# Optimization experiments

Hardware: AMD Instinct MI355X
Metric: run time of the kernel (lower is better)

## Reference

```python
import jax, jax.numpy as jnp
import numpy as np

EMB = 512
HEADS = 8
HEAD_DIM = EMB // HEADS
GN_EPS = 1e-6
THETA_SCALE = 10000.0


def _multiply_by_i(x):
    # interleave: out[..., 2i] = -x[..., 2i+1], out[..., 2i+1] = x[..., 2i]
    return jnp.stack((-x[..., 1::2], x[..., ::2]), axis=-1).reshape(x.shape)


def _theta_shift(x, sin, cos):
    return x * cos + _multiply_by_i(x) * sin


def setup_inputs() -> dict:
    key = jax.random.key(0)
    ks = jax.random.split(key, 13)
    B, N, E = 2, 2048, EMB

    def xavier(k, out_dim, in_dim):
        std = (2.0 / (out_dim + in_dim)) ** 0.5
        return std * jax.random.normal(k, (out_dim, in_dim), dtype=jnp.float32)

    return {
        "query": jax.random.normal(ks[0], (B, N, E), dtype=jnp.float32),
        "k": jax.random.normal(ks[1], (B, N, E), dtype=jnp.float32),
        "v": jax.random.normal(ks[2], (B, N, E), dtype=jnp.float32),
        "Wq": xavier(ks[3], E, E), "bq": jnp.zeros((E,), jnp.float32),
        "Wk": xavier(ks[4], E, E), "bk": jnp.zeros((E,), jnp.float32),
        "Wv": xavier(ks[5], E, E), "bv": jnp.zeros((E,), jnp.float32),
        "Wg": xavier(ks[6], E, E), "bg": jnp.zeros((E,), jnp.float32),
        "Wo": xavier(ks[7], E, E), "bo": jnp.zeros((E,), jnp.float32),
    }


def reference(query, k, v, Wq, bq, Wk, bk, Wv, bv, Wg, bg, Wo, bo):
    B, N, E = query.shape
    H, D = HEADS, E // HEADS

    def proj(x, W, b):  # torch Linear: x @ W.T + b, then split heads -> [b h n d]
        return (x @ W.T + b).reshape(B, N, H, D).transpose(0, 2, 1, 3)

    q = proj(query, Wq, bq)
    kk = proj(k, Wk, bk)
    vv = proj(v, Wv, bv)

    # rotary-style theta shift; thetas repeated pairwise [t0,t0,t1,t1,...]
    thetas = jnp.repeat(1.0 / THETA_SCALE ** jnp.linspace(0.0, 1.0, D // 2), 2)
    angles = jnp.arange(N, dtype=jnp.float32)[:, None] * thetas[None, :]  # [n d]
    sin = jnp.sin(angles)[None, None]
    cos = jnp.cos(angles)[None, None]
    q = _theta_shift(q, sin, cos)
    kk = _theta_shift(kk, sin, cos)

    # decay-masked retention (softmax-free)
    gammas = 1.0 - jnp.exp(jnp.linspace(np.log(1 / 32), np.log(1 / 512), H)).astype(jnp.float32)
    pos = jnp.arange(N)
    dist = jnp.abs(pos[:, None] - pos[None, :]).astype(jnp.float32)
    causal = pos[:, None] >= pos[None, :]
    decay_mask = jnp.where(causal[None], gammas[:, None, None] ** dist[None], 0.0)  # [h n s]

    kk = kk / (D ** 0.5)
    sim = jnp.einsum('bhnd,bhsd->bhns', q, kk) * decay_mask[None]  # [b h n n]
    ret = jnp.einsum('bhns,bhsd->bhnd', sim, vv)

    # GroupNorm(groups=H, channels=H, affine=False) over (b n) samples -> per-(b,h,n) norm over d
    mean = ret.mean(axis=-1, keepdims=True)
    var = ret.var(axis=-1, keepdims=True)
    ret = (ret - mean) / jnp.sqrt(var + GN_EPS)

    ret = ret.transpose(0, 2, 1, 3).reshape(B, N, E)
    gate = jax.nn.silu(query @ Wg.T + bg)
    out = (ret * gate) @ Wo.T + bo
    return out
```

## Files before the change

kernel.cpp:

```cpp
#include <hip/hip_runtime.h>
#include <math.h>

typedef float f32x4 __attribute__((ext_vector_type(4)));
typedef short s16x8 __attribute__((ext_vector_type(8)));
typedef short s16x4 __attribute__((ext_vector_type(4)));

__device__ __forceinline__ short f2bf(float f) {
    unsigned u = __builtin_bit_cast(unsigned, f);
    unsigned r = u + 0x7FFFu + ((u >> 16) & 1u);
    return (short)(r >> 16);
}
__device__ __forceinline__ float bf2f(short h) {
    return __builtin_bit_cast(float, ((unsigned)(unsigned short)h) << 16);
}
__device__ __forceinline__ unsigned pack2(short a, short b) {
    return (unsigned)(unsigned short)a | ((unsigned)(unsigned short)b << 16);
}

__device__ __forceinline__ void split16v(const float* __restrict__ p,
                                         short* __restrict__ h,
                                         short* __restrict__ l) {
    f32x4 a0 = *(const f32x4*)(p);
    f32x4 a1 = *(const f32x4*)(p + 4);
    f32x4 a2 = *(const f32x4*)(p + 8);
    f32x4 a3 = *(const f32x4*)(p + 12);
    #pragma unroll
    for (int i = 0; i < 4; ++i) {
        short t0;
        t0 = f2bf(a0[i]); h[i]      = t0; l[i]      = f2bf(a0[i] - bf2f(t0));
        t0 = f2bf(a1[i]); h[4 + i]  = t0; l[4 + i]  = f2bf(a1[i] - bf2f(t0));
        t0 = f2bf(a2[i]); h[8 + i]  = t0; l[8 + i]  = f2bf(a2[i] - bf2f(t0));
        t0 = f2bf(a3[i]); h[12 + i] = t0; l[12 + i] = f2bf(a3[i] - bf2f(t0));
    }
}

__device__ __forceinline__ void gload16(const void* g, void* l) {
    __builtin_amdgcn_global_load_lds(
        (const __attribute__((address_space(1))) unsigned int*)g,
        (__attribute__((address_space(3))) unsigned int*)l,
        16, 0, 0);
}

__global__ __launch_bounds__(256) void presplit_kernel(
    const float* __restrict__ W0, const float* __restrict__ W1,
    const float* __restrict__ W2, const float* __restrict__ W3,
    const float* __restrict__ W4,
    const float* __restrict__ X0, const float* __restrict__ X1,
    const float* __restrict__ X2,
    short* __restrict__ Wsp, short* __restrict__ Xsp,
    float2* __restrict__ SC)
{
    const int blk = blockIdx.x;
    const int t = threadIdx.x;
    short hbuf[16], lbuf[16];
    if (blk < 256) {
        const int w = blk >> 6, bi = blk & 63;
        const float* src = (w == 0) ? W0 : (w == 1) ? W1 : (w == 2) ? W2 : W3;
        const int idx = (bi * 256 + t) * 16;
        const int row = idx >> 9, k0 = idx & 511;
        const int ntile = row >> 7, r = row & 127;
        const int kstep = k0 >> 5, kk0 = k0 & 31;
        const int s = (r & 3) << 4;
        split16v(src + idx, hbuf, lbuf);
        short* hp = Wsp + (long)w * 524288 + (ntile * 16 + kstep) * 8192 + r * 32;
        short* lp = hp + 4096;
        const int oA = ((2 * kk0) ^ s) >> 1;
        const int oB = ((2 * kk0 + 16) ^ s) >> 1;
        *(s16x8*)(hp + oA) = *(s16x8*)(hbuf);
        *(s16x8*)(hp + oB) = *(s16x8*)(hbuf + 8);
        *(s16x8*)(lp + oA) = *(s16x8*)(lbuf);
        *(s16x8*)(lp + oB) = *(s16x8*)(lbuf + 8);
    } else if (blk < 320) {
        const int bi = blk - 256;
        const int idx = (bi * 256 + t) * 16;
        short* hi = Wsp + (long)4 * 524288;
        short* lo = hi + 262144;
        split16v(W4 + idx, hbuf, lbuf);
        *(s16x8*)(hi + idx)     = *(s16x8*)(hbuf);
        *(s16x8*)(hi + idx + 8) = *(s16x8*)(hbuf + 8);
        *(s16x8*)(lo + idx)     = *(s16x8*)(lbuf);
        *(s16x8*)(lo + idx + 8) = *(s16x8*)(lbuf + 8);
    } else if (blk < 1856) {
        const int b2 = blk - 320;
        const int x = b2 >> 9, bi = b2 & 511;
        const float* src = (x == 0) ? X0 : (x == 1) ? X1 : X2;
        const int idx = (bi * 256 + t) * 16;
        const int row = idx >> 9, k0 = idx & 511;
        const int mtile = row >> 6, r = row & 63;
        const int kstep = k0 >> 5, kk0 = k0 & 31;
        const int s = (r & 3) << 4;
        split16v(src + idx, hbuf, lbuf);
        short* hp = Xsp + (long)x * 4194304 + (mtile * 16 + kstep) * 4096 + r * 32;
        short* lp = hp + 2048;
        const int oA = ((2 * kk0) ^ s) >> 1;
        const int oB = ((2 * kk0 + 16) ^ s) >> 1;
        *(s16x8*)(hp + oA) = *(s16x8*)(hbuf);
        *(s16x8*)(hp + oB) = *(s16x8*)(hbuf + 8);
        *(s16x8*)(lp + oA) = *(s16x8*)(lbuf);
        *(s16x8*)(lp + oB) = *(s16x8*)(lbuf + 8);
    } else {
        const int gid = (blk - 1856) * 256 + t;
        const int pos = gid >> 5, pp = gid & 31;
        const float theta = powf(10000.0f, -(float)pp * (1.0f / 31.0f));
        const float ang = (float)pos * theta;
        SC[gid] = make_float2(cosf(ang), sinf(ang));
    }
}

__global__ __launch_bounds__(512, 4) void projqkvg_kernel(
    const short* __restrict__ Xsp, const short* __restrict__ Wsp,
    const float* __restrict__ bq, const float* __restrict__ bk,
    const float* __restrict__ bv, const float* __restrict__ bg,
    const float2* __restrict__ SC,
    short* __restrict__ Qh, short* __restrict__ Ql,
    short* __restrict__ Kh, short* __restrict__ Vth,
    float* __restrict__ G)
{
    __shared__ __align__(16) short SB[36864];

    const int fid = blockIdx.x + 4 * (blockIdx.y + 64 * blockIdx.z);
    const int mtile = fid & 63;
    const int rr = fid >> 6;
    const int mode = rr & 3;
    const int ntile = rr >> 2;
    const int m0 = mtile * 64, n0 = ntile * 128;

    const int xi = (mode == 1) ? 1 : (mode == 2) ? 2 : 0;
    const float* bias = (mode == 0) ? bq : (mode == 1) ? bk
                       : (mode == 2) ? bv : bg;

    const int t = threadIdx.x, lane = t & 63, wv = t >> 6;
    const int wm = wv >> 2, wn = wv & 3;
    const int quad = lane >> 4, l15 = lane & 15;

    const short* Xblk = Xsp + (long)xi * 4194304 + (long)mtile * 16 * 4096;
    const short* Wblk = Wsp + (long)mode * 524288 + (long)ntile * 16 * 8192;

    const int c0 = wv * 3;
    const short* gs[3];
    int gstp[3];
    #pragma unroll
    for (int i = 0; i < 3; ++i) {
        const int c = c0 + i;
        const bool isx = (c < 8);
        gs[i]   = isx ? (Xblk + c * 512 + lane * 8)
                      : (Wblk + (c - 8) * 512 + lane * 8);
        gstp[i] = isx ? 4096 : 8192;
    }

    auto STAGE = [&](int stg, int ks) {
        char* dstb = (char*)SB + stg * 24576 + c0 * 1024;
        #pragma unroll
        for (int i = 0; i < 3; ++i)
            gload16(gs[i] + ks * gstp[i], dstb + i * 1024);
    };

    const int sxw = (l15 & 3) << 4;
    int aoff[2], boff[2];
    #pragma unroll
    for (int s2 = 0; s2 < 2; ++s2)
        aoff[s2] = (wm * 32 + s2 * 16 + l15) * 64 + ((quad * 16) ^ sxw);
    #pragma unroll
    for (int s2 = 0; s2 < 2; ++s2)
        boff[s2] = 8192 + (wn * 32 + s2 * 16 + l15) * 64 + ((quad * 16) ^ sxw);

    f32x4 acc[2][2];
    #pragma unroll
    for (int i = 0; i < 2; ++i)
        #pragma unroll
        for (int j = 0; j < 2; ++j)
            acc[i][j] = (f32x4){0.f, 0.f, 0.f, 0.f};

    STAGE(0, 0);
    STAGE(1, 1);
    asm volatile("s_waitcnt vmcnt(3)" ::: "memory");
    __builtin_amdgcn_s_barrier();

    int cur = 0;
    for (int ks = 0; ks < 16; ++ks) {
        if (ks < 14) {
            int fill = cur + 2; if (fill >= 3) fill -= 3;
            STAGE(fill, ks + 2);
        }
        __builtin_amdgcn_sched_barrier(0);

        const char* stg = (const char*)SB + cur * 24576;
        s16x8 ah[2], al[2], bh[2], bl[2];
        #pragma unroll
        for (int s2 = 0; s2 < 2; ++s2) {
            ah[s2] = *(const s16x8*)(stg + aoff[s2]);
            al[s2] = *(const s16x8*)(stg + 4096 + aoff[s2]);
        }
        #pragma unroll
        for (int s2 = 0; s2 < 2; ++s2) {
            bh[s2] = *(const s16x8*)(stg + boff[s2]);
            bl[s2] = *(const s16x8*)(stg + 8192 + boff[s2]);
        }
        __builtin_amdgcn_s_setprio(1);
        #pragma unroll
        for (int i = 0; i < 2; ++i)
            #pragma unroll
            for (int j = 0; j < 2; ++j) {
                acc[i][j] = __builtin_amdgcn_mfma_f32_16x16x32_bf16(ah[i], bh[j], acc[i][j], 0, 0, 0);
                acc[i][j] = __builtin_amdgcn_mfma_f32_16x16x32_bf16(al[i], bh[j], acc[i][j], 0, 0, 0);
                acc[i][j] = __builtin_amdgcn_mfma_f32_16x16x32_bf16(ah[i], bl[j], acc[i][j], 0, 0, 0);
            }
        __builtin_amdgcn_s_setprio(0);

        if (ks < 14)       asm volatile("s_waitcnt vmcnt(3)" ::: "memory");
        else if (ks == 14) asm volatile("s_waitcnt vmcnt(0)" ::: "memory");
        __builtin_amdgcn_sched_barrier(0);
        __builtin_amdgcn_s_barrier();

        cur += 1; if (cur >= 3) cur -= 3;
    }

    __syncthreads();

    const int bb = m0 >> 11, posb = m0 & 2047;

    if (mode == 0) {
        short* Thi = SB + wv * 1280;
        short* Tlo = Thi + 640;
        const int head = (n0 >> 6) + (wn >> 1);
        const int dbase = (wn & 1) * 32;
        #pragma unroll
        for (int ms = 0; ms < 2; ++ms) {
            #pragma unroll
            for (int ns = 0; ns < 2; ++ns) {
                const int col = n0 + wn * 32 + ns * 16 + l15;
                const float bvv = bias[col];
                const int pp = (col & 63) >> 1;
                #pragma unroll
                for (int r = 0; r < 4; ++r) {
                    const int m = m0 + wm * 32 + ms * 16 + quad * 4 + r;
                    const int pos = m & 2047;
                    float x = acc[ms][ns][r] + bvv;
                    float prt = __shfl_xor(x, 1);
                    float2 sc = SC[pos * 32 + pp];
                    float y0 = x * sc.x - prt * sc.y;
                    float y1 = prt * sc.x + x * sc.y;
                    if (!(l15 & 1)) {
                        short h0 = f2bf(y0), h1 = f2bf(y1);
                        short l0 = f2bf(y0 - bf2f(h0)), l1 = f2bf(y1 - bf2f(h1));
                        const int o = (quad * 4 + r) * 40 + ns * 16 + l15;
                        *(unsigned*)&Thi[o] = pack2(h0, h1);
                        *(unsigned*)&Tlo[o] = pack2(l0, l1);
                    }
                }
            }
            const int mrow = wm * 32 + ms * 16;
            const int row = lane >> 2, ch = (lane & 3) * 8;
            s16x8 vh = *(const s16x8*)&Thi[row * 40 + ch];
            s16x8 vl = *(const s16x8*)&Tlo[row * 40 + ch];
            const long o = ((long)(bb * 8 + head) * 2048 + posb + mrow + row) * 64 + dbase + ch;
            *(s16x8*)(Qh + o) = vh;
            *(s16x8*)(Ql + o) = vl;
        }
    } else if (mode == 1) {
        short* Thi = SB + wv * 640;
        const int head = (n0 >> 6) + (wn >> 1);
        const int dbase = (wn & 1) * 32;
        #pragma unroll
        for (int ms = 0; ms < 2; ++ms) {
            #pragma unroll
            for (int ns = 0; ns < 2; ++ns) {
                const int col = n0 + wn * 32 + ns * 16 + l15;
                const float bvv = bias[col];
                const int pp = (col & 63) >> 1;
                #pragma unroll
                for (int r = 0; r < 4; ++r) {
                    const int m = m0 + wm * 32 + ms * 16 + quad * 4 + r;
                    const int pos = m & 2047;
                    float x = acc[ms][ns][r] + bvv;
                    float prt = __shfl_xor(x, 1);
                    float2 sc = SC[pos * 32 + pp];
                    float y0 = (x * sc.x - prt * sc.y) * 0.125f;
                    float y1 = (prt * sc.x + x * sc.y) * 0.125f;
                    if (!(l15 & 1)) {
                        const int o = (quad * 4 + r) * 40 + ns * 16 + l15;
                        *(unsigned*)&Thi[o] = pack2(f2bf(y0), f2bf(y1));
                    }
                }
            }
            const int mrow = wm * 32 + ms * 16;
            const int row = lane >> 2, ch = (lane & 3) * 8;
            s16x8 vh = *(const s16x8*)&Thi[row * 40 + ch];
            const long o = ((long)(bb * 8 + head) * 2048 + posb + mrow + row) * 64 + dbase + ch;
            *(s16x8*)(Kh + o) = vh;
        }
    } else if (mode == 2) {
        short* T2 = SB;
        #pragma unroll
        for (int ns = 0; ns < 2; ++ns) {
            const int col = n0 + wn * 32 + ns * 16 + l15;
            const float bvv = bias[col];
            #pragma unroll
            for (int ms = 0; ms < 2; ++ms) {
                s16x4 pk;
                #pragma unroll
                for (int r = 0; r < 4; ++r)
                    pk[r] = f2bf(acc[ms][ns][r] + bvv);
                *(s16x4*)&T2[(wn * 32 + ns * 16 + l15) * 72
                             + wm * 32 + ms * 16 + quad * 4] = pk;
            }
        }
        __syncthreads();
        #pragma unroll
        for (int pass = 0; pass < 2; ++pass) {
            const int row = pass * 64 + (t >> 3);
            const int ch = (t & 7) * 8;
            s16x8 v = *(const s16x8*)&T2[row * 72 + ch];
            const int head = (n0 >> 6) + (row >> 6);
            const int d = row & 63;
            const long o = ((long)(bb * 8 + head) * 64 + d) * 2048 + posb + ch;
            *(s16x8*)(Vth + o) = v;
        }
    } else {
        #pragma unroll
        for (int ns = 0; ns < 2; ++ns) {
            const int col = n0 + wn * 32 + ns * 16 + l15;
            const float bvv = bias[col];
            #pragma unroll
            for (int ms = 0; ms < 2; ++ms)
                #pragma unroll
                for (int r = 0; r < 4; ++r) {
                    const int m = m0 + wm * 32 + ms * 16 + quad * 4 + r;
                    float x = acc[ms][ns][r] + bvv;
                    G[(long)m * 512 + col] = x / (1.0f + expf(-x));
                }
        }
    }
}

__global__ __launch_bounds__(256) void attn_kernel(
    const short* __restrict__ Qh_g, const short* __restrict__ Ql_g,
    const short* __restrict__ Kh_g, const short* __restrict__ Vth_g,
    const float* __restrict__ G,
    short* __restrict__ RGh)
{
    __shared__ __align__(16) short KhS[64 * 72], VhS[64 * 72];
    __shared__ __align__(16) short PhS[64 * 68];

    const int t = threadIdx.x, lane = t & 63, wv = t >> 6;
    const int quad = lane >> 4, l15 = lane & 15;
    const int bh = blockIdx.y, h = bh & 7, b = bh >> 3;
    const int qt = (bh & 1) ? blockIdx.x : (31 - blockIdx.x);
    const int n0 = qt * 64;
    const long base = (long)bh * 2048 * 64;

    float l2g;
    int stLo;
    {
        float lg0 = logf(1.0f / 32.0f), lg1 = logf(1.0f / 512.0f);
        float om = expf(lg0 + (float)h * (lg1 - lg0) * (1.0f / 7.0f));
        l2g = log2f(1.0f - om);
        int Dcut = (int)(11.5129255f / om) + 64;
        stLo = (n0 - Dcut) >> 6;
        if (stLo < 0) stLo = 0;
    }
    float gneg[16];
    #pragma unroll
    for (int i = 0; i < 16; ++i)
        gneg[i] = exp2f(-(float)((i >> 2) * 16 + (i & 3)) * l2g);

    const int srow = t >> 2;
    const int scol = (t & 3) * 16;
    const int n = n0 + wv * 16 + l15;

    s16x8 qh[2], ql[2];
    {
        const short* qp  = Qh_g + base + (long)(n0 + wv * 16 + l15) * 64 + quad * 8;
        const short* qp2 = Ql_g + base + (long)(n0 + wv * 16 + l15) * 64 + quad * 8;
        qh[0] = *(const s16x8*)qp;
        qh[1] = *(const s16x8*)(qp + 32);
        ql[0] = *(const s16x8*)qp2;
        ql[1] = *(const s16x8*)(qp2 + 32);
    }

    f32x4 racc[4];
    #pragma unroll
    for (int i = 0; i < 4; ++i) racc[i] = (f32x4){0.f, 0.f, 0.f, 0.f};

    s16x8 pk0, pk1, pv0, pv1;
    {
        const long ko = base + (long)(stLo * 64 + srow) * 64 + scol;
        pk0 = *(const s16x8*)(Kh_g + ko);
        pk1 = *(const s16x8*)(Kh_g + ko + 8);
        const long vo = base + (long)srow * 2048 + stLo * 64 + scol;
        pv0 = *(const s16x8*)(Vth_g + vo);
        pv1 = *(const s16x8*)(Vth_g + vo + 8);
    }

    for (int st = stLo; st <= qt; ++st) {
        const int s0 = st * 64;
        __syncthreads();
        *(s16x8*)&KhS[srow * 72 + scol]     = pk0;
        *(s16x8*)&KhS[srow * 72 + scol + 8] = pk1;
        *(s16x8*)&VhS[srow * 72 + scol]     = pv0;
        *(s16x8*)&VhS[srow * 72 + scol + 8] = pv1;
        __syncthreads();

        if (st < qt) {
            const long ko = base + (long)(s0 + 64 + srow) * 64 + scol;
            pk0 = *(const s16x8*)(Kh_g + ko);
            pk1 = *(const s16x8*)(Kh_g + ko + 8);
            const long vo = base + (long)srow * 2048 + s0 + 64 + scol;
            pv0 = *(const s16x8*)(Vth_g + vo);
            pv1 = *(const s16x8*)(Vth_g + vo + 8);
        }

        const float t0 = exp2f((float)(n - s0 - quad * 4) * l2g);

        #pragma unroll
        for (int sub = 0; sub < 4; ++sub) {
            const int ro = (sub * 16 + l15) * 72 + quad * 8;
            s16x8 kh0 = *(const s16x8*)&KhS[ro];
            s16x8 kh1 = *(const s16x8*)&KhS[ro + 32];
            f32x4 sacc = (f32x4){0.f, 0.f, 0.f, 0.f};
            sacc = __builtin_amdgcn_mfma_f32_16x16x32_bf16(kh0, qh[0], sacc, 0, 0, 0);
            sacc = __builtin_amdgcn_mfma_f32_16x16x32_bf16(kh1, qh[1], sacc, 0, 0, 0);
            sacc = __builtin_amdgcn_mfma_f32_16x16x32_bf16(kh0, ql[0], sacc, 0, 0, 0);
            sacc = __builtin_amdgcn_mfma_f32_16x16x32_bf16(kh1, ql[1], sacc, 0, 0, 0);

            const int sb = s0 + sub * 16 + quad * 4;
            s16x4 pkh;
            #pragma unroll
            for (int r = 0; r < 4; ++r) {
                const int s = sb + r;
                const float wgt = (n >= s) ? t0 * gneg[sub * 4 + r] : 0.0f;
                pkh[r] = f2bf(sacc[r] * wgt);
            }
            *(s16x4*)&PhS[(wv * 16 + l15) * 68 + sub * 16 + quad * 4] = pkh;
        }

        const int pro = (wv * 16 + l15) * 68 + quad * 8;
        s16x8 ph0 = *(const s16x8*)&PhS[pro];
        s16x8 ph1 = *(const s16x8*)&PhS[pro + 32];
        #pragma unroll
        for (int ds = 0; ds < 4; ++ds) {
            const int ro = (ds * 16 + l15) * 72 + quad * 8;
            s16x8 vh0 = *(const s16x8*)&VhS[ro];
            s16x8 vh1 = *(const s16x8*)&VhS[ro + 32];
            racc[ds] = __builtin_amdgcn_mfma_f32_16x16x32_bf16(ph0, vh0, racc[ds], 0, 0, 0);
            racc[ds] = __builtin_amdgcn_mfma_f32_16x16x32_bf16(ph1, vh1, racc[ds], 0, 0, 0);
        }
    }

    float mean[4], rstd[4];
    #pragma unroll
    for (int r = 0; r < 4; ++r) {
        float s = racc[0][r] + racc[1][r] + racc[2][r] + racc[3][r];
        s += __shfl_xor(s, 1); s += __shfl_xor(s, 2);
        s += __shfl_xor(s, 4); s += __shfl_xor(s, 8);
        mean[r] = s * (1.0f / 64.0f);
        float vs = 0.f;
        #pragma unroll
        for (int ds = 0; ds < 4; ++ds) {
            float d = racc[ds][r] - mean[r];
            vs += d * d;
        }
        vs += __shfl_xor(vs, 1); vs += __shfl_xor(vs, 2);
        vs += __shfl_xor(vs, 4); vs += __shfl_xor(vs, 8);
        rstd[r] = rsqrtf(vs * (1.0f / 64.0f) + 1e-6f);
    }

    __syncthreads();
    short* rgH = KhS + wv * 1152;
    #pragma unroll
    for (int ds = 0; ds < 4; ++ds) {
        #pragma unroll
        for (int r = 0; r < 4; ++r) {
            const int nn = n0 + wv * 16 + quad * 4 + r;
            const int d = ds * 16 + l15;
            const long gi = ((long)(b * 2048 + nn)) * 512 + h * 64 + d;
            float rg = (racc[ds][r] - mean[r]) * rstd[r] * G[gi];
            float prt = __shfl_xor(rg, 1);
            if (!(l15 & 1)) {
                const int o = (quad * 4 + r) * 72 + ds * 16 + l15;
                *(unsigned*)&rgH[o] = pack2(f2bf(rg), f2bf(prt));
            }
        }
    }
    #pragma unroll
    for (int p2 = 0; p2 < 2; ++p2) {
        const int row = p2 * 8 + (lane >> 3);
        const int ch = (lane & 7) * 8;
        s16x8 vh = *(const s16x8*)&rgH[row * 72 + ch];
        const int nn = n0 + wv * 16 + row;
        const long o = ((long)(b * 2048 + nn)) * 512 + h * 64 + ch;
        *(s16x8*)(RGh + o) = vh;
    }
}

__global__ __launch_bounds__(256) void projo_kernel(
    const short* __restrict__ RGh, const short* __restrict__ Woh_g,
    const float* __restrict__ bo, float* __restrict__ out)
{
    __shared__ __align__(16) char PB[23040];
    short* XhS = (short*)PB;
    short* WhS = XhS + 1280;
    short* WlS = XhS + 6400;

    const short* Wol_g = Woh_g + 262144;
    const int t = threadIdx.x, lane = t & 63, wv = t >> 6;
    const int wm = wv >> 1, wn = wv & 1;
    const int quad = lane >> 4, l15 = lane & 15;
    const int m0 = blockIdx.y * 32, n0 = blockIdx.x * 128;

    f32x4 acc[4];
    #pragma unroll
    for (int j = 0; j < 4; ++j) acc[j] = (f32x4){0.f, 0.f, 0.f, 0.f};

    const int xrow = t >> 3, xcol = (t & 7) * 4;
    const int wrow = t >> 1, wcol = (t & 1) * 16;
    const long xbase = (long)(m0 + xrow) * 512 + xcol;
    const long wbase = (long)(n0 + wrow) * 512 + wcol;

    s16x4 px;
    s16x8 pw0, pw1, pw2, pw3;
    px  = *(const s16x4*)(RGh + xbase);
    pw0 = *(const s16x8*)(Woh_g + wbase);
    pw1 = *(const s16x8*)(Woh_g + wbase + 8);
    pw2 = *(const s16x8*)(Wol_g + wbase);
    pw3 = *(const s16x8*)(Wol_g + wbase + 8);

    for (int k0 = 0; k0 < 512; k0 += 32) {
        __syncthreads();
        *(s16x4*)&XhS[xrow * 40 + xcol]     = px;
        *(s16x8*)&WhS[wrow * 40 + wcol]     = pw0;
        *(s16x8*)&WhS[wrow * 40 + wcol + 8] = pw1;
        *(s16x8*)&WlS[wrow * 40 + wcol]     = pw2;
        *(s16x8*)&WlS[wrow * 40 + wcol + 8] = pw3;
        __syncthreads();

        if (k0 + 32 < 512) {
            const long xo = xbase + k0 + 32;
            const long wo = wbase + k0 + 32;
            px  = *(const s16x4*)(RGh + xo);
            pw0 = *(const s16x8*)(Woh_g + wo);
            pw1 = *(const s16x8*)(Woh_g + wo + 8);
            pw2 = *(const s16x8*)(Wol_g + wo);
            pw3 = *(const s16x8*)(Wol_g + wo + 8);
        }

        s16x8 ah, bh[4], bl[4];
        {
            const int ro = (wm * 16 + l15) * 40 + quad * 8;
            ah = *(const s16x8*)&XhS[ro];
        }
        #pragma unroll
        for (int s = 0; s < 4; ++s) {
            const int ro = (wn * 64 + s * 16 + l15) * 40 + quad * 8;
            bh[s] = *(const s16x8*)&WhS[ro];
            bl[s] = *(const s16x8*)&WlS[ro];
        }
        #pragma unroll
        for (int j = 0; j < 4; ++j) {
            acc[j] = __builtin_amdgcn_mfma_f32_16x16x32_bf16(ah, bh[j], acc[j], 0, 0, 0);
            acc[j] = __builtin_amdgcn_mfma_f32_16x16x32_bf16(ah, bl[j], acc[j], 0, 0, 0);
        }
    }

    __syncthreads();
    float* T = (float*)PB + wv * 1152;
    #pragma unroll
    for (int ns = 0; ns < 4; ++ns) {
        const int col = n0 + wn * 64 + ns * 16 + l15;
        const float bvv = bo[col];
        #pragma unroll
        for (int r = 0; r < 4; ++r)
            T[(quad * 4 + r) * 72 + ns * 16 + l15] = acc[ns][r] + bvv;
    }
    #pragma unroll
    for (int it = 0; it < 2; ++it) {
        const int row = it * 8 + (lane >> 3);
        const int ch = (lane & 7) * 8;
        f32x4 a = *(const f32x4*)&T[row * 72 + ch];
        f32x4 c = *(const f32x4*)&T[row * 72 + ch + 4];
        const long o = (long)(m0 + wm * 16 + row) * 512 + n0 + wn * 64 + ch;
        *(f32x4*)(out + o) = a;
        *(f32x4*)(out + o + 4) = c;
    }
}

extern "C" void kernel_launch(void* const* d_in, const int* in_sizes, int n_in,
                              void* d_out, int out_size, void* d_ws, size_t ws_size,
                              hipStream_t stream) {
    const float* query = (const float*)d_in[0];
    const float* kin   = (const float*)d_in[1];
    const float* vin   = (const float*)d_in[2];
    const float* Wq = (const float*)d_in[3];
    const float* bq = (const float*)d_in[4];
    const float* Wk = (const float*)d_in[5];
    const float* bk = (const float*)d_in[6];
    const float* Wv = (const float*)d_in[7];
    const float* bv = (const float*)d_in[8];
    const float* Wg = (const float*)d_in[9];
    const float* bg = (const float*)d_in[10];
    const float* Wo = (const float*)d_in[11];
    const float* bo = (const float*)d_in[12];

    short* S = (short*)d_ws;
    const long NE = 2097152;
    short* WSp = S;
    short* Xsp = S + 2621440;
    short* Qh  = Xsp + 12582912;
    short* Ql  = Qh + NE;
    short* Kh  = Ql + NE;
    short* Vth = Kh + NE;
    float* G   = (float*)(Vth + NE);
    short* RGh = (short*)(G + NE);
    float2* SC = (float2*)(RGh + NE);

    presplit_kernel<<<2112, 256, 0, stream>>>(
        Wq, Wk, Wv, Wg, Wo, query, kin, vin, WSp, Xsp, SC);
    projqkvg_kernel<<<dim3(4, 64, 4), 512, 0, stream>>>(
        Xsp, WSp, bq, bk, bv, bg, SC, Qh, Ql, Kh, Vth, G);
    attn_kernel<<<dim3(32, 16), 256, 0, stream>>>(
        Qh, Ql, Kh, Vth, G, RGh);
    projo_kernel<<<dim3(4, 128), 256, 0, stream>>>(
        RGh, WSp + 4 * 524288, bo, (float*)d_out);
}
```

Measured before the change: 194.5 us.

## Split attention key tiles across two wave groups per block

Doubles the attention block to 512 threads, forming two groups of four waves. Each group processes alternating key/value tiles with its own shared-memory buffers, and the partial retention accumulators are then reduced through shared memory before the group norm and gating. The aim is more parallelism per query tile and shorter serial loops over the decay window. The cost is more shared memory per block, an extra reduction step, and idle waves when a tile count is odd.

```diff
diff --git a/kernel.cpp b/kernel.cpp
--- a/kernel.cpp
+++ b/kernel.cpp
@@ -333,16 +333,19 @@
     }
 }
 
-__global__ __launch_bounds__(256) void attn_kernel(
+__global__ __launch_bounds__(512) void attn_kernel(
     const short* __restrict__ Qh_g, const short* __restrict__ Ql_g,
     const short* __restrict__ Kh_g, const short* __restrict__ Vth_g,
     const float* __restrict__ G,
     short* __restrict__ RGh)
 {
-    __shared__ __align__(16) short KhS[64 * 72], VhS[64 * 72];
-    __shared__ __align__(16) short PhS[64 * 68];
+    __shared__ __align__(16) short KhS[2][4608];
+    __shared__ __align__(16) short VhS[2][4608];
+    __shared__ __align__(16) short PhS[2][4352];
 
     const int t = threadIdx.x, lane = t & 63, wv = t >> 6;
+    const int grp = wv >> 2, wq = wv & 3;
+    const int tg = t & 255;
     const int quad = lane >> 4, l15 = lane & 15;
     const int bh = blockIdx.y, h = bh & 7, b = bh >> 3;
     const int qt = (bh & 1) ? blockIdx.x : (31 - blockIdx.x);
@@ -364,14 +367,18 @@
     for (int i = 0; i < 16; ++i)
         gneg[i] = exp2f(-(float)((i >> 2) * 16 + (i & 3)) * l2g);
 
-    const int srow = t >> 2;
-    const int scol = (t & 3) * 16;
-    const int n = n0 + wv * 16 + l15;
+    short* khs = KhS[grp];
+    short* vhs = VhS[grp];
+    short* phs = PhS[grp];
+
+    const int srow = tg >> 2;
+    const int scol = (tg & 3) * 16;
+    const int n = n0 + wq * 16 + l15;
 
     s16x8 qh[2], ql[2];
     {
-        const short* qp  = Qh_g + base + (long)(n0 + wv * 16 + l15) * 64 + quad * 8;
-        const short* qp2 = Ql_g + base + (long)(n0 + wv * 16 + l15) * 64 + quad * 8;
+        const short* qp  = Qh_g + base + (long)(n0 + wq * 16 + l15) * 64 + quad * 8;
+        const short* qp2 = Ql_g + base + (long)(n0 + wq * 16 + l15) * 64 + quad * 8;
         qh[0] = *(const s16x8*)qp;
         qh[1] = *(const s16x8*)(qp + 32);
         ql[0] = *(const s16x8*)qp2;
@@ -382,114 +389,138 @@
     #pragma unroll
     for (int i = 0; i < 4; ++i) racc[i] = (f32x4){0.f, 0.f, 0.f, 0.f};
 
+    const int ntiles = qt - stLo + 1;
+    const int nIter = (ntiles + 1) >> 1;
+    int st = stLo + grp;
+
     s16x8 pk0, pk1, pv0, pv1;
     {
-        const long ko = base + (long)(stLo * 64 + srow) * 64 + scol;
+        const int stc = (st <= qt) ? st : qt;
+        const long ko = base + (long)(stc * 64 + srow) * 64 + scol;
         pk0 = *(const s16x8*)(Kh_g + ko);
         pk1 = *(const s16x8*)(Kh_g + ko + 8);
-        const long vo = base + (long)srow * 2048 + stLo * 64 + scol;
+        const long vo = base + (long)srow * 2048 + stc * 64 + scol;
         pv0 = *(const s16x8*)(Vth_g + vo);
         pv1 = *(const s16x8*)(Vth_g + vo + 8);
     }
 
-    for (int st = stLo; st <= qt; ++st) {
-        const int s0 = st * 64;
+    for (int i = 0; i < nIter; ++i, st += 2) {
         __syncthreads();
-        *(s16x8*)&KhS[srow * 72 + scol]     = pk0;
-        *(s16x8*)&KhS[srow * 72 + scol + 8] = pk1;
-        *(s16x8*)&VhS[srow * 72 + scol]     = pv0;
-        *(s16x8*)&VhS[srow * 72 + scol + 8] = pv1;
+        *(s16x8*)&khs[srow * 72 + scol]     = pk0;
+        *(s16x8*)&khs[srow * 72 + scol + 8] = pk1;
+        *(s16x8*)&vhs[srow * 72 + scol]     = pv0;
+        *(s16x8*)&vhs[srow * 72 + scol + 8] = pv1;
         __syncthreads();
 
-        if (st < qt) {
-            const long ko = base + (long)(s0 + 64 + srow) * 64 + scol;
+        if (st + 2 <= qt) {
+            const long ko = base + (long)((st + 2) * 64 + srow) * 64 + scol;
             pk0 = *(const s16x8*)(Kh_g + ko);
             pk1 = *(const s16x8*)(Kh_g + ko + 8);
-            const long vo = base + (long)srow * 2048 + s0 + 64 + scol;
+            const long vo = base + (long)srow * 2048 + (st + 2) * 64 + scol;
             pv0 = *(const s16x8*)(Vth_g + vo);
             pv1 = *(const s16x8*)(Vth_g + vo + 8);
         }
 
-        const float t0 = exp2f((float)(n - s0 - quad * 4) * l2g);
-
-        #pragma unroll
-        for (int sub = 0; sub < 4; ++sub) {
-            const int ro = (sub * 16 + l15) * 72 + quad * 8;
-            s16x8 kh0 = *(const s16x8*)&KhS[ro];
-            s16x8 kh1 = *(const s16x8*)&KhS[ro + 32];
-            f32x4 sacc = (f32x4){0.f, 0.f, 0.f, 0.f};
-            sacc = __builtin_amdgcn_mfma_f32_16x16x32_bf16(kh0, qh[0], sacc, 0, 0, 0);
-            sacc = __builtin_amdgcn_mfma_f32_16x16x32_bf16(kh1, qh[1], sacc, 0, 0, 0);
-            sacc = __builtin_amdgcn_mfma_f32_16x16x32_bf16(kh0, ql[0], sacc, 0, 0, 0);
-            sacc = __builtin_amdgcn_mfma_f32_16x16x32_bf16(kh1, ql[1], sacc, 0, 0, 0);
-
-            const int sb = s0 + sub * 16 + quad * 4;
-            s16x4 pkh;
+        if (st <= qt) {
+            const int s0 = st * 64;
+            const float t0 = exp2f((float)(n - s0 - quad * 4) * l2g);
+
+            #pragma unroll
+            for (int sub = 0; sub < 4; ++sub) {
+                const int ro = (sub * 16 + l15) * 72 + quad * 8;
+                s16x8 kh0 = *(const s16x8*)&khs[ro];
+                s16x8 kh1 = *(const s16x8*)&khs[ro + 32];
+                f32x4 sacc = (f32x4){0.f, 0.f, 0.f, 0.f};
+                sacc = __builtin_amdgcn_mfma_f32_16x16x32_bf16(kh0, qh[0], sacc, 0, 0, 0);
+                sacc = __builtin_amdgcn_mfma_f32_16x16x32_bf16(kh1, qh[1], sacc, 0, 0, 0);
+                sacc = __builtin_amdgcn_mfma_f32_16x16x32_bf16(kh0, ql[0], sacc, 0, 0, 0);
+                sacc = __builtin_amdgcn_mfma_f32_16x16x32_bf16(kh1, ql[1], sacc, 0, 0, 0);
+
+                const int sb = s0 + sub * 16 + quad * 4;
+                s16x4 pkh;
+                #pragma unroll
+                for (int r = 0; r < 4; ++r) {
+                    const int s = sb + r;
+                    const float wgt = (n >= s) ? t0 * gneg[sub * 4 + r] : 0.0f;
+                    pkh[r] = f2bf(sacc[r] * wgt);
+                }
+                *(s16x4*)&phs[(wq * 16 + l15) * 68 + sub * 16 + quad * 4] = pkh;
+            }
+
+            const int pro = (wq * 16 + l15) * 68 + quad * 8;
+            s16x8 ph0 = *(const s16x8*)&phs[pro];
+            s16x8 ph1 = *(const s16x8*)&phs[pro + 32];
+            #pragma unroll
+            for (int ds = 0; ds < 4; ++ds) {
+                const int ro = (ds * 16 + l15) * 72 + quad * 8;
+                s16x8 vh0 = *(const s16x8*)&vhs[ro];
+                s16x8 vh1 = *(const s16x8*)&vhs[ro + 32];
+                racc[ds] = __builtin_amdgcn_mfma_f32_16x16x32_bf16(ph0, vh0, racc[ds], 0, 0, 0);
+                racc[ds] = __builtin_amdgcn_mfma_f32_16x16x32_bf16(ph1, vh1, racc[ds], 0, 0, 0);
+            }
+        }
+    }
+
+    __syncthreads();
+    float* R = (float*)KhS;
+    if (grp == 1) {
+        #pragma unroll
+        for (int ds = 0; ds < 4; ++ds)
+            #pragma unroll
+            for (int r = 0; r < 4; ++r)
+                R[(wq * 16 + quad * 4 + r) * 68 + ds * 16 + l15] = racc[ds][r];
+    }
+    __syncthreads();
+    if (grp == 0) {
+        #pragma unroll
+        for (int ds = 0; ds < 4; ++ds)
+            #pragma unroll
+            for (int r = 0; r < 4; ++r)
+                racc[ds][r] += R[(wq * 16 + quad * 4 + r) * 68 + ds * 16 + l15];
+
+        float mean[4], rstd[4];
+        #pragma unroll
+        for (int r = 0; r < 4; ++r) {
+            float s = racc[0][r] + racc[1][r] + racc[2][r] + racc[3][r];
+            s += __shfl_xor(s, 1); s += __shfl_xor(s, 2);
+            s += __shfl_xor(s, 4); s += __shfl_xor(s, 8);
+            mean[r] = s * (1.0f / 64.0f);
+            float vs = 0.f;
+            #pragma unroll
+            for (int ds = 0; ds < 4; ++ds) {
+                float d = racc[ds][r] - mean[r];
+                vs += d * d;
+            }
+            vs += __shfl_xor(vs, 1); vs += __shfl_xor(vs, 2);
+            vs += __shfl_xor(vs, 4); vs += __shfl_xor(vs, 8);
+            rstd[r] = rsqrtf(vs * (1.0f / 64.0f) + 1e-6f);
+        }
+
+        short* rgH = (short*)PhS + wq * 1152;
+        #pragma unroll
+        for (int ds = 0; ds < 4; ++ds) {
             #pragma unroll
             for (int r = 0; r < 4; ++r) {
-                const int s = sb + r;
-                const float wgt = (n >= s) ? t0 * gneg[sub * 4 + r] : 0.0f;
-                pkh[r] = f2bf(sacc[r] * wgt);
-            }
-            *(s16x4*)&PhS[(wv * 16 + l15) * 68 + sub * 16 + quad * 4] = pkh;
-        }
-
-        const int pro = (wv * 16 + l15) * 68 + quad * 8;
-        s16x8 ph0 = *(const s16x8*)&PhS[pro];
-        s16x8 ph1 = *(const s16x8*)&PhS[pro + 32];
-        #pragma unroll
-        for (int ds = 0; ds < 4; ++ds) {
-            const int ro = (ds * 16 + l15) * 72 + quad * 8;
-            s16x8 vh0 = *(const s16x8*)&VhS[ro];
-            s16x8 vh1 = *(const s16x8*)&VhS[ro + 32];
-            racc[ds] = __builtin_amdgcn_mfma_f32_16x16x32_bf16(ph0, vh0, racc[ds], 0, 0, 0);
-            racc[ds] = __builtin_amdgcn_mfma_f32_16x16x32_bf16(ph1, vh1, racc[ds], 0, 0, 0);
-        }
-    }
-
-    float mean[4], rstd[4];
-    #pragma unroll
-    for (int r = 0; r < 4; ++r) {
-        float s = racc[0][r] + racc[1][r] + racc[2][r] + racc[3][r];
-        s += __shfl_xor(s, 1); s += __shfl_xor(s, 2);
-        s += __shfl_xor(s, 4); s += __shfl_xor(s, 8);
-        mean[r] = s * (1.0f / 64.0f);
-        float vs = 0.f;
-        #pragma unroll
-        for (int ds = 0; ds < 4; ++ds) {
-            float d = racc[ds][r] - mean[r];
-            vs += d * d;
-        }
-        vs += __shfl_xor(vs, 1); vs += __shfl_xor(vs, 2);
-        vs += __shfl_xor(vs, 4); vs += __shfl_xor(vs, 8);
-        rstd[r] = rsqrtf(vs * (1.0f / 64.0f) + 1e-6f);
-    }
-
-    __syncthreads();
-    short* rgH = KhS + wv * 1152;
-    #pragma unroll
-    for (int ds = 0; ds < 4; ++ds) {
-        #pragma unroll
-        for (int r = 0; r < 4; ++r) {
-            const int nn = n0 + wv * 16 + quad * 4 + r;
-            const int d = ds * 16 + l15;
-            const long gi = ((long)(b * 2048 + nn)) * 512 + h * 64 + d;
-            float rg = (racc[ds][r] - mean[r]) * rstd[r] * G[gi];
-            float prt = __shfl_xor(rg, 1);
-            if (!(l15 & 1)) {
-                const int o = (quad * 4 + r) * 72 + ds * 16 + l15;
-                *(unsigned*)&rgH[o] = pack2(f2bf(rg), f2bf(prt));
-            }
-        }
-    }
-    #pragma unroll
-    for (int p2 = 0; p2 < 2; ++p2) {
-        const int row = p2 * 8 + (lane >> 3);
-        const int ch = (lane & 7) * 8;
-        s16x8 vh = *(const s16x8*)&rgH[row * 72 + ch];
-        const int nn = n0 + wv * 16 + row;
-        const long o = ((long)(b * 2048 + nn)) * 512 + h * 64 + ch;
-        *(s16x8*)(RGh + o) = vh;
+                const int nn = n0 + wq * 16 + quad * 4 + r;
+                const int d = ds * 16 + l15;
+                const long gi = ((long)(b * 2048 + nn)) * 512 + h * 64 + d;
+                float rg = (racc[ds][r] - mean[r]) * rstd[r] * G[gi];
+                float prt = __shfl_xor(rg, 1);
+                if (!(l15 & 1)) {
+                    const int o = (quad * 4 + r) * 72 + ds * 16 + l15;
+                    *(unsigned*)&rgH[o] = pack2(f2bf(rg), f2bf(prt));
+                }
+            }
+        }
+        #pragma unroll
+        for (int p2 = 0; p2 < 2; ++p2) {
+            const int row = p2 * 8 + (lane >> 3);
+            const int ch = (lane & 7) * 8;
+            s16x8 vh = *(const s16x8*)&rgH[row * 72 + ch];
+            const int nn = n0 + wq * 16 + row;
+            const long o = ((long)(b * 2048 + nn)) * 512 + h * 64 + ch;
+            *(s16x8*)(RGh + o) = vh;
+        }
     }
 }
 
@@ -617,7 +648,7 @@
         Wq, Wk, Wv, Wg, Wo, query, kin, vin, WSp, Xsp, SC);
     projqkvg_kernel<<<dim3(4, 64, 4), 512, 0, stream>>>(
         Xsp, WSp, bq, bk, bv, bg, SC, Qh, Ql, Kh, Vth, G);
-    attn_kernel<<<dim3(32, 16), 256, 0, stream>>>(
+    attn_kernel<<<dim3(32, 16), 512, 0, stream>>>(
         Qh, Ql, Kh, Vth, G, RGh);
     projo_kernel<<<dim3(4, 128), 256, 0, stream>>>(
         RGh, WSp + 4 * 524288, bo, (float*)d_out);
```

After: 198.9 us. 1.02x slower.

## Split attention over key-tile chunks with a separate reduce-and-normalize kernel

Applied to the files above, without the earlier changes.

The retention kernel now splits each query tile's key range into up to two chunks of 16 key tiles. Each chunk block writes its fp32 partial accumulator to scratch reused from the split-input buffer, and a new finish kernel sums the partials and applies the GroupNorm, gate and bf16 pack. The aim is to balance the uneven per-tile work, since long-decay heads span many key tiles, and to expose more blocks. The cost is an extra launch, a round trip of partials through global memory, and blocks that exit early when their chunk is empty.

```diff
diff --git a/kernel.cpp b/kernel.cpp
--- a/kernel.cpp
+++ b/kernel.cpp
@@ -39,6 +39,15 @@
         (const __attribute__((address_space(1))) unsigned int*)g,
         (__attribute__((address_space(3))) unsigned int*)l,
         16, 0, 0);
+}
+
+__device__ __forceinline__ void decay_params(int h, int n0, float& l2g, int& stLo) {
+    float lg0 = logf(1.0f / 32.0f), lg1 = logf(1.0f / 512.0f);
+    float om = expf(lg0 + (float)h * (lg1 - lg0) * (1.0f / 7.0f));
+    l2g = log2f(1.0f - om);
+    int Dcut = (int)(11.5129255f / om) + 64;
+    stLo = (n0 - Dcut) >> 6;
+    if (stLo < 0) stLo = 0;
 }
 
 __global__ __launch_bounds__(256) void presplit_kernel(
@@ -333,32 +342,33 @@
     }
 }
 
-__global__ __launch_bounds__(256) void attn_kernel(
+__global__ __launch_bounds__(256) void attn_chunk_kernel(
     const short* __restrict__ Qh_g, const short* __restrict__ Ql_g,
     const short* __restrict__ Kh_g, const short* __restrict__ Vth_g,
-    const float* __restrict__ G,
-    short* __restrict__ RGh)
+    float* __restrict__ Racc)
 {
     __shared__ __align__(16) short KhS[64 * 72], VhS[64 * 72];
     __shared__ __align__(16) short PhS[64 * 68];
 
+    const int fid = blockIdx.x;
+    const int bh = fid & 15;
+    const int rest = fid >> 4;
+    const int qt = rest & 31;
+    const int c  = rest >> 5;
+    const int h = bh & 7;
+    const int n0 = qt * 64;
+
+    float l2g;
+    int stLo;
+    decay_params(h, n0, l2g, stLo);
+    const int st0 = stLo + c * 16;
+    if (st0 > qt) return;
+    const int stHi = min(st0 + 15, qt);
+
     const int t = threadIdx.x, lane = t & 63, wv = t >> 6;
     const int quad = lane >> 4, l15 = lane & 15;
-    const int bh = blockIdx.y, h = bh & 7, b = bh >> 3;
-    const int qt = (bh & 1) ? blockIdx.x : (31 - blockIdx.x);
-    const int n0 = qt * 64;
     const long base = (long)bh * 2048 * 64;
 
-    float l2g;
-    int stLo;
-    {
-        float lg0 = logf(1.0f / 32.0f), lg1 = logf(1.0f / 512.0f);
-        float om = expf(lg0 + (float)h * (lg1 - lg0) * (1.0f / 7.0f));
-        l2g = log2f(1.0f - om);
-        int Dcut = (int)(11.5129255f / om) + 64;
-        stLo = (n0 - Dcut) >> 6;
-        if (stLo < 0) stLo = 0;
-    }
     float gneg[16];
     #pragma unroll
     for (int i = 0; i < 16; ++i)
@@ -384,15 +394,15 @@
 
     s16x8 pk0, pk1, pv0, pv1;
     {
-        const long ko = base + (long)(stLo * 64 + srow) * 64 + scol;
+        const long ko = base + (long)(st0 * 64 + srow) * 64 + scol;
         pk0 = *(const s16x8*)(Kh_g + ko);
         pk1 = *(const s16x8*)(Kh_g + ko + 8);
-        const long vo = base + (long)srow * 2048 + stLo * 64 + scol;
+        const long vo = base + (long)srow * 2048 + st0 * 64 + scol;
         pv0 = *(const s16x8*)(Vth_g + vo);
         pv1 = *(const s16x8*)(Vth_g + vo + 8);
     }
 
-    for (int st = stLo; st <= qt; ++st) {
+    for (int st = st0; st <= stHi; ++st) {
         const int s0 = st * 64;
         __syncthreads();
         *(s16x8*)&KhS[srow * 72 + scol]     = pk0;
@@ -401,11 +411,11 @@
         *(s16x8*)&VhS[srow * 72 + scol + 8] = pv1;
         __syncthreads();
 
-        if (st < qt) {
-            const long ko = base + (long)(s0 + 64 + srow) * 64 + scol;
+        if (st < stHi) {
+            const long ko = base + (long)((st + 1) * 64 + srow) * 64 + scol;
             pk0 = *(const s16x8*)(Kh_g + ko);
             pk1 = *(const s16x8*)(Kh_g + ko + 8);
-            const long vo = base + (long)srow * 2048 + s0 + 64 + scol;
+            const long vo = base + (long)srow * 2048 + (st + 1) * 64 + scol;
             pv0 = *(const s16x8*)(Vth_g + vo);
             pv1 = *(const s16x8*)(Vth_g + vo + 8);
         }
@@ -447,6 +457,47 @@
         }
     }
 
+    float* dst = Racc + (long)((bh * 32 + qt) * 2 + c) * 4096;
+    #pragma unroll
+    for (int ds = 0; ds < 4; ++ds)
+        #pragma unroll
+        for (int r = 0; r < 4; ++r)
+            dst[(wv * 16 + quad * 4 + r) * 64 + ds * 16 + l15] = racc[ds][r];
+}
+
+__global__ __launch_bounds__(256) void attn_finish_kernel(
+    const float* __restrict__ Racc, const float* __restrict__ G,
+    short* __restrict__ RGh)
+{
+    __shared__ __align__(16) short rgS[4608];
+
+    const int fid = blockIdx.x;
+    const int bh = fid & 15;
+    const int qt = fid >> 4;
+    const int h = bh & 7, b = bh >> 3;
+    const int n0 = qt * 64;
+
+    float l2g;
+    int stLo;
+    decay_params(h, n0, l2g, stLo);
+    const int ntiles = qt - stLo + 1;
+    const int nc = (ntiles + 15) >> 4;
+
+    const int t = threadIdx.x, lane = t & 63, wv = t >> 6;
+    const int quad = lane >> 4, l15 = lane & 15;
+
+    const float* s0 = Racc + (long)((bh * 32 + qt) * 2) * 4096;
+    f32x4 racc[4];
+    #pragma unroll
+    for (int ds = 0; ds < 4; ++ds)
+        #pragma unroll
+        for (int r = 0; r < 4; ++r) {
+            const int o = (wv * 16 + quad * 4 + r) * 64 + ds * 16 + l15;
+            float v = s0[o];
+            if (nc > 1) v += s0[4096 + o];
+            racc[ds][r] = v;
+        }
+
     float mean[4], rstd[4];
     #pragma unroll
     for (int r = 0; r < 4; ++r) {
@@ -465,8 +516,7 @@
         rstd[r] = rsqrtf(vs * (1.0f / 64.0f) + 1e-6f);
     }
 
-    __syncthreads();
-    short* rgH = KhS + wv * 1152;
+    short* rgH = rgS + wv * 1152;
     #pragma unroll
     for (int ds = 0; ds < 4; ++ds) {
         #pragma unroll
@@ -482,6 +532,7 @@
             }
         }
     }
+    __syncthreads();
     #pragma unroll
     for (int p2 = 0; p2 < 2; ++p2) {
         const int row = p2 * 8 + (lane >> 3);
@@ -612,13 +663,16 @@
     float* G   = (float*)(Vth + NE);
     short* RGh = (short*)(G + NE);
     float2* SC = (float2*)(RGh + NE);
+    float* Racc = (float*)Xsp;
 
     presplit_kernel<<<2112, 256, 0, stream>>>(
         Wq, Wk, Wv, Wg, Wo, query, kin, vin, WSp, Xsp, SC);
     projqkvg_kernel<<<dim3(4, 64, 4), 512, 0, stream>>>(
         Xsp, WSp, bq, bk, bv, bg, SC, Qh, Ql, Kh, Vth, G);
-    attn_kernel<<<dim3(32, 16), 256, 0, stream>>>(
-        Qh, Ql, Kh, Vth, G, RGh);
+    attn_chunk_kernel<<<1024, 256, 0, stream>>>(
+        Qh, Ql, Kh, Vth, Racc);
+    attn_finish_kernel<<<512, 256, 0, stream>>>(
+        Racc, G, RGh);
     projo_kernel<<<dim3(4, 128), 256, 0, stream>>>(
         RGh, WSp + 4 * 524288, bo, (float*)d_out);
 }
```

After: 192.3 us. About the same (-1.1%).
